# Kernel tuning notes

Measured on AMD Instinct MI355X. Metric: run time of the kernel, lower is better.

Reference implementation:

```python
import jax, jax.numpy as jnp
from jax import lax
import numpy as np

DN = ('NCDHW', 'OIDHW', 'NCDHW')
SLOPE = 0.01   # nn.LeakyReLU default negative_slope
EPS = 1e-5     # nn.BatchNorm1d default eps


def _conv(x, w, s, p):
    return lax.conv_general_dilated(x, w, (s, s, s), [(p, p)] * 3,
                                    dimension_numbers=DN)


def _tconv(x, w):
    # ConvTranspose3d(k=4, s=2, p=1) == conv with lhs_dilation=2,
    # pad = k-1-p = 2, spatially flipped kernel. w is (C_out, C_in, 4,4,4).
    return lax.conv_general_dilated(x, jnp.flip(w, (2, 3, 4)), (1, 1, 1),
                                    [(2, 2)] * 3, lhs_dilation=(2, 2, 2),
                                    dimension_numbers=DN)


def _bcast(v):
    return v[None, :, None, None, None]


def _masked_bn(y, m, g, b):
    # BatchNorm1d over ACTIVE voxels only (spconv stores only active sites).
    cnt = jnp.maximum(jnp.sum(m), 1.0)
    mean = jnp.sum(y * m, axis=(0, 2, 3, 4)) / cnt
    var = jnp.sum(jnp.square(y - _bcast(mean)) * m, axis=(0, 2, 3, 4)) / cnt
    yhat = (y - _bcast(mean)) * _bcast(lax.rsqrt(var + EPS))
    return (yhat * _bcast(g) + _bcast(b)) * m


def _block(x, m, w, b, g, be, transpose):
    # spconv SparseConv(Transpose)3d -> LeakyReLU -> BatchNorm1d, emulated
    # densely: x is zero off the active set m; output active set is the
    # dilation of m by the kernel footprint; bias/activation/BN touch only
    # active sites.
    ones_k = jnp.ones((1, 1, 4, 4, 4), x.dtype)
    if transpose:
        y = _tconv(x, w)
        m2 = (_tconv(m, ones_k) > 0).astype(x.dtype)
    else:
        y = _conv(x, w, 2, 1)
        m2 = (_conv(m, ones_k, 2, 1) > 0).astype(x.dtype)
    y = (y + _bcast(b)) * m2
    y = jnp.where(y >= 0, y, SLOPE * y)  # LeakyReLU (preserves zeros)
    return _masked_bn(y, m2, g, be), m2


def setup_inputs() -> dict:
    key = jax.random.key(0)
    ks = jax.random.split(key, 16)
    B, C, D = 2, 4, 64
    c = 32          # chans
    pred_dim = 32

    def w_init(k, shape):
        scale = 1.0 / float(np.sqrt(np.prod(shape[1:])))
        return jax.random.normal(k, shape, jnp.float32) * scale

    def b_init(k, n):
        return jax.random.normal(k, (n,), jnp.float32) * 0.01

    inp = {
        'feat': jax.random.normal(ks[0], (B, C, D, D, D), jnp.float32),
        'mask': jax.random.uniform(ks[1], (B, 1, D, D, D), jnp.float32),
        # down: [C->c, c->2c, 2c->4c], k=4 s=2 p=1
        'w1': w_init(ks[2], (c, C, 4, 4, 4)),
        'b1': b_init(ks[3], c),
        'g1': jnp.ones((c,), jnp.float32), 'be1': jnp.zeros((c,), jnp.float32),
        'w2': w_init(ks[4], (2 * c, c, 4, 4, 4)),
        'b2': b_init(ks[5], 2 * c),
        'g2': jnp.ones((2 * c,), jnp.float32), 'be2': jnp.zeros((2 * c,), jnp.float32),
        'w3': w_init(ks[6], (4 * c, 2 * c, 4, 4, 4)),
        'b3': b_init(ks[7], 4 * c),
        'g3': jnp.ones((4 * c,), jnp.float32), 'be3': jnp.zeros((4 * c,), jnp.float32),
        # up: [4c->4c, 4c->2c] (no skip-concat in the executed forward)
        'tw1': w_init(ks[8], (4 * c, 4 * c, 4, 4, 4)),
        'tb1': b_init(ks[9], 4 * c),
        'tg1': jnp.ones((4 * c,), jnp.float32), 'tbe1': jnp.zeros((4 * c,), jnp.float32),
        'tw2': w_init(ks[10], (2 * c, 4 * c, 4, 4, 4)),
        'tb2': b_init(ks[11], 2 * c),
        'tg2': jnp.ones((2 * c,), jnp.float32), 'tbe2': jnp.zeros((2 * c,), jnp.float32),
        # final dense 1x1x1 Conv3d: 2c -> pred_dim
        'fw': w_init(ks[12], (pred_dim, 2 * c, 1, 1, 1)),
        'fb': b_init(ks[13], pred_dim),
    }
    return inp


def reference(feat, mask, w1, b1, g1, be1, w2, b2, g2, be2, w3, b3, g3, be3,
              tw1, tb1, tg1, tbe1, tw2, tb2, tg2, tbe2, fw, fb):
    m = (mask > 0.5).astype(feat.dtype)
    x = feat * m  # gather of active voxel features == dense zero-fill
    x, m = _block(x, m, w1, b1, g1, be1, False)   # 64^3 -> 32^3
    x, m = _block(x, m, w2, b2, g2, be2, False)   # 32^3 -> 16^3
    x, m = _block(x, m, w3, b3, g3, be3, False)   # 16^3 -> 8^3
    x, m = _block(x, m, tw1, tb1, tg1, tbe1, True)  # 8^3 -> 16^3
    x, m = _block(x, m, tw2, tb2, tg2, tbe2, True)  # 16^3 -> 32^3
    # ToDense() then dense 1x1x1 Conv3d (bias applied everywhere)
    return _conv(x, fw, 1, 0) + _bcast(fb)
```

## Files before the change

### kernel.cpp

```cpp
#include <hip/hip_runtime.h>
#include <hip/hip_bf16.h>

#define DEV static __device__ __forceinline__

typedef unsigned short ushort;
typedef __attribute__((ext_vector_type(8))) short short8;
typedef __attribute__((ext_vector_type(8))) ushort ushort8;
typedef __attribute__((ext_vector_type(4))) ushort ushortx4;
typedef __attribute__((ext_vector_type(4))) float accv;

DEV ushort f2bf(float f) {
    __hip_bfloat16 h = __float2bfloat16(f);
    return reinterpret_cast<ushort&>(h);
}

__device__ float    g_sred[5 * 128 * 32];
__device__ float    g_part1[128 * 96];
__device__ float    g_part5[64 * 192];
__device__ float    g_y1[2097152];
__device__ __align__(16) ushort g_y1b[2097152];
__device__ float    g_m1[65536];
__device__ float    g_y2[524288];
__device__ __align__(16) ushort g_y2b[524288];
__device__ float    g_m2[8192];
__device__ float    g_y3[131072];
__device__ __align__(16) ushort g_y3b[131072];
__device__ float    g_m3[1024];
__device__ float    g_t1[1048576];
__device__ __align__(16) ushort g_t1b[1048576];
__device__ float    g_mt1[8192];
__device__ float    g_mt2[65536];
__device__ float    g_t2[4194304];
__device__ __align__(16) ushort g_x0b[2097152];
__device__ float    g_p2[4194304];
__device__ float    g_p3[4194304];
__device__ float    g_p4[8388608];
__device__ __align__(16) ushort g_wb1[8192];
__device__ __align__(16) ushort g_wb2[131072];
__device__ __align__(16) ushort g_wb3[524288];
__device__ __align__(16) ushort g_wb4[1048576];
__device__ __align__(16) ushort g_wb5[524288];
__device__ float    g_fwt[2048];

__global__ __launch_bounds__(256)
void prep_all_kernel(const float* __restrict__ w1, const float* __restrict__ fw,
                     const float* __restrict__ w2, const float* __restrict__ w3,
                     const float* __restrict__ tw1, const float* __restrict__ tw2,
                     const float* __restrict__ feat, const float* __restrict__ mask) {
    int blk = blockIdx.x, tid = threadIdx.x;
    if (blk < 96) {
        int idx = blk * 256 + tid;
        if (idx < 20480) g_sred[idx] = 0.f;
        if (idx < 12288) g_part1[idx] = 0.f;
        if (idx < 12288) g_part5[idx] = 0.f;
        if (idx < 8192) {
            int co = idx >> 8, r = idx & 255;
            int tap = r >> 2, ci = r & 3;
            g_wb1[idx] = f2bf(w1[co * 256 + ci * 64 + tap]);
        }
        if (idx < 2048) { int co = idx >> 6, kg = idx & 63; g_fwt[kg * 32 + co] = fw[idx]; }
    } else if (blk < 608) {
        int idx = (blk - 96) * 256 + tid;
        int co = idx / 2048, r = idx % 2048;
        int ci = r >> 6, tap = r & 63;
        g_wb2[(size_t)co * 2048 + tap * 32 + ci] = f2bf(w2[idx]);
    } else if (blk < 2656) {
        int idx = (blk - 608) * 256 + tid;
        int co = idx / 4096, r = idx % 4096;
        int ci = r >> 6, tap = r & 63;
        g_wb3[(size_t)co * 4096 + tap * 64 + ci] = f2bf(w3[idx]);
    } else if (blk < 6752) {
        int idx = (blk - 2656) * 256 + tid;
        int co = idx / 8192, r = idx % 8192;
        int ci = r >> 6, t64 = r & 63;
        int kd = t64 >> 4, kh = (t64 >> 2) & 3, kw = t64 & 3;
        int pd = (3 - kd) & 1, td = (3 - kd) >> 1;
        int ph = (3 - kh) & 1, th = (3 - kh) >> 1;
        int pw = (3 - kw) & 1, tw = (3 - kw) >> 1;
        int parity = pd * 4 + ph * 2 + pw, t = td * 4 + th * 2 + tw;
        g_wb4[(((size_t)parity * 128 + co) * 8 + t) * 128 + ci] = f2bf(tw1[idx]);
    } else if (blk < 8800) {
        int idx = (blk - 6752) * 256 + tid;
        int co = idx / 8192, r = idx % 8192;
        int ci = r >> 6, t64 = r & 63;
        int kd = t64 >> 4, kh = (t64 >> 2) & 3, kw = t64 & 3;
        int pd = (3 - kd) & 1, td = (3 - kd) >> 1;
        int ph = (3 - kh) & 1, th = (3 - kh) >> 1;
        int pw = (3 - kw) & 1, tw = (3 - kw) >> 1;
        int parity = pd * 4 + ph * 2 + pw, t = td * 4 + th * 2 + tw;
        g_wb5[(((size_t)parity * 64 + co) * 8 + t) * 128 + ci] = f2bf(tw2[idx]);
    } else if (blk < 10848) {
        int idx = (blk - 8800) * 256 + tid;
        int b = idx >> 18, v = idx & 0x3FFFF;
        float mv = mask[idx] > 0.5f ? 1.f : 0.f;
        ushort pk[4];
#pragma unroll
        for (int c = 0; c < 4; c++) pk[c] = f2bf(feat[((b * 4 + c) << 18) + v] * mv);
        *(ushortx4*)&g_x0b[(size_t)idx * 4] = (ushortx4){pk[0], pk[1], pk[2], pk[3]};
    } else {
        int idx = (blk - 10848) * 256 + tid;
        int b = idx >> 15, v = idx & 0x7FFF;
        int od = v >> 10, rem = v & 1023;
        int oh = rem >> 5, ow = rem & 31;
        const float* mp = mask + ((size_t)b << 18);
        float acc = 0.f;
        for (int kd = 0; kd < 4; kd++) {
            int id = 2 * od - 1 + kd;
            if ((unsigned)id >= 64u) continue;
            for (int kh = 0; kh < 4; kh++) {
                int ih = 2 * oh - 1 + kh;
                if ((unsigned)ih >= 64u) continue;
                const float* row = mp + ((size_t)id * 64 + ih) * 64;
                for (int kw = 0; kw < 4; kw++) {
                    int iw = 2 * ow - 1 + kw;
                    if ((unsigned)iw < 64u && row[iw] > 0.5f) acc += 1.f;
                }
            }
        }
        g_m1[idx] = acc > 0.f ? 1.f : 0.f;
    }
}

DEV void mask_down_blk(const float* mprev, float* mout, int logDin, int logDo, int blk) {
    int Din = 1 << logDin, Do = 1 << logDo;
    int idx = blk * 256 + threadIdx.x;
    int b = idx >> (3 * logDo), v = idx & ((1 << (3 * logDo)) - 1);
    int od = v >> (2 * logDo), rem = v & ((1 << (2 * logDo)) - 1);
    int oh = rem >> logDo, ow = rem & (Do - 1);
    const float* mp = mprev + ((size_t)b << (3 * logDin));
    float acc = 0.f;
    for (int kd = 0; kd < 4; kd++) {
        int id = 2 * od - 1 + kd;
        if ((unsigned)id >= (unsigned)Din) continue;
        for (int kh = 0; kh < 4; kh++) {
            int ih = 2 * oh - 1 + kh;
            if ((unsigned)ih >= (unsigned)Din) continue;
            const float* row = mp + ((size_t)id * Din + ih) * Din;
            for (int kw = 0; kw < 4; kw++) {
                int iw = 2 * ow - 1 + kw;
                if ((unsigned)iw < (unsigned)Din) acc += row[iw];
            }
        }
    }
    mout[idx] = acc > 0.f ? 1.f : 0.f;
}

DEV void mask_up_blk(const float* mprev, float* mout, int logDin, int logDo, int blk) {
    int Din = 1 << logDin, Do = 1 << logDo;
    int idx = blk * 256 + threadIdx.x;
    int b = idx >> (3 * logDo), v = idx & ((1 << (3 * logDo)) - 1);
    int od = v >> (2 * logDo), rem = v & ((1 << (2 * logDo)) - 1);
    int oh = rem >> logDo, ow = rem & (Do - 1);
    const float* mp = mprev + ((size_t)b << (3 * logDin));
    float acc = 0.f;
    for (int kd = 0; kd < 4; kd++) {
        int u = od + kd - 2; if (u < 0 || (u & 1)) continue;
        int id = u >> 1; if (id >= Din) continue;
        for (int kh = 0; kh < 4; kh++) {
            int uh = oh + kh - 2; if (uh < 0 || (uh & 1)) continue;
            int ih = uh >> 1; if (ih >= Din) continue;
            const float* row = mp + ((size_t)id * Din + ih) * Din;
            for (int kw = 0; kw < 4; kw++) {
                int uw = ow + kw - 2; if (uw < 0 || (uw & 1)) continue;
                int iw = uw >> 1; if (iw >= Din) continue;
                acc += row[iw];
            }
        }
    }
    mout[idx] = acc > 0.f ? 1.f : 0.f;
}

template<int MODE, int MT, int NT, int CIN, int COUT, int LOGDI, int LOGDO, int SPLITK,
         int KT, bool STATS = false>
DEV void mfma_gemm_body(const ushort* __restrict__ xb, const ushort* __restrict__ wb,
                        float* __restrict__ y,
                        const float* __restrict__ bias = nullptr,
                        const float* __restrict__ m2 = nullptr,
                        float* __restrict__ part = nullptr) {
    constexpr int K  = (MODE == 1) ? CIN * 8 : CIN * 64;
    constexpr int KSEG = K / SPLITK;
    constexpr int OCT = KT / 8;
    constexpr int LOGOCT = (KT == 32) ? 2 : 3;
    constexpr int KKN = KT / 32;
    constexpr int LDA = KT + 8;
    constexpr int MTW = MT / 32, NTW = NT / 32;
    constexpr int AR = MT * OCT / 256, BR = NT * OCT / 256;
    constexpr int LCIN = (CIN == 32) ? 5 : ((CIN == 64) ? 6 : 7);
    constexpr int Din = 1 << LOGDI, Do = 1 << LOGDO;
    constexpr int DvoxI = 1 << (3 * LOGDI), DvoxO = 1 << (3 * LOGDO);

    __shared__ __align__(16) ushort As[2][MT * LDA];
    __shared__ __align__(16) ushort Bs[2][NT * LDA];
    __shared__ float st[STATS ? COUT * 3 : 1];

    const int tid = threadIdx.x;
    const int bx = blockIdx.x;
    int pd = 0, ph = 0, pw = 0, ks = 0;
    const ushort* wp = wb;
    if constexpr (MODE == 1) {
        int z = blockIdx.z;
        pd = (z >> 2) & 1; ph = (z >> 1) & 1; pw = z & 1; ks = z >> 3;
        wp = wb + (size_t)(z & 7) * COUT * CIN * 8;
    } else {
        ks = blockIdx.z;
    }

    const int wv = tid >> 6, lane = tid & 63;
    const int mw = wv & 1, nw = wv >> 1;
    const int lr = lane & 15, quad = lane >> 4;

    if constexpr (STATS) {
        for (int i = tid; i < COUT * 3; i += 256) st[i] = 0.f;
    }

    int rB[BR], dB[BR], hB[BR], wBv[BR];
#pragma unroll
    for (int r = 0; r < BR; r++) {
        int slot = r * 256 + tid;
        int n = slot >> LOGOCT;
        int vg = bx * NT + n;
        if constexpr (MODE == 0) {
            rB[r] = vg >> (3 * LOGDO);
            int vv = vg & (DvoxO - 1);
            dB[r] = 2 * (vv >> (2 * LOGDO)) - 1;
            hB[r] = 2 * ((vv >> LOGDO) & (Do - 1)) - 1;
            wBv[r] = 2 * (vv & (Do - 1)) - 1;
        } else {
            rB[r] = vg >> (3 * LOGDI);
            int vv = vg & (DvoxI - 1);
            dB[r] = (vv >> (2 * LOGDI)) + pd - 1;
            hB[r] = ((vv >> LOGDI) & (Din - 1)) + ph - 1;
            wBv[r] = (vv & (Din - 1)) + pw - 1;
        }
    }

    auto gatherA = [&](int kt, ushort8* pa) {
#pragma unroll
        for (int r = 0; r < AR; r++) {
            int slot = r * 256 + tid;
            int m = slot >> LOGOCT, oct = slot & (OCT - 1);
            pa[r] = *(const ushort8*)&wp[(size_t)m * K + kt + oct * 8];
        }
    };
    auto gatherB = [&](int kt, ushort8* pb) {
#pragma unroll
        for (int r = 0; r < BR; r++) {
            int oct = (r * 256 + tid) & (OCT - 1);
            int kk0 = kt + oct * 8;
            int tap = kk0 >> LCIN;
            int ci0 = kk0 & (CIN - 1);
            int id_d, ih_d, iw_d;
            if constexpr (MODE == 0) { id_d = tap >> 4; ih_d = (tap >> 2) & 3; iw_d = tap & 3; }
            else                     { id_d = (tap >> 2) & 1; ih_d = (tap >> 1) & 1; iw_d = tap & 1; }
            int id = dB[r] + id_d, ih = hB[r] + ih_d, iw = wBv[r] + iw_d;
            ushort8 v = (ushort8){0, 0, 0, 0, 0, 0, 0, 0};
            if ((unsigned)id < (unsigned)Din && (unsigned)ih < (unsigned)Din &&
                (unsigned)iw < (unsigned)Din)
                v = *(const ushort8*)&xb[((size_t)rB[r] * DvoxI +
                                          (id << (2 * LOGDI)) + (ih << LOGDI) + iw) * CIN + ci0];
            pb[r] = v;
        }
    };
    auto stage = [&](int buf, ushort8* a, ushort8* b) {
#pragma unroll
        for (int r = 0; r < AR; r++) {
            int slot = r * 256 + tid;
            int m = slot >> LOGOCT, oct = slot & (OCT - 1);
            *(ushort8*)&As[buf][m * LDA + oct * 8] = a[r];
        }
#pragma unroll
        for (int r = 0; r < BR; r++) {
            int slot = r * 256 + tid;
            int n = slot >> LOGOCT, oct = slot & (OCT - 1);
            *(ushort8*)&Bs[buf][n * LDA + oct * 8] = b[r];
        }
    };

    accv acc[MTW][NTW];
#pragma unroll
    for (int mt = 0; mt < MTW; mt++)
#pragma unroll
        for (int nt = 0; nt < NTW; nt++) acc[mt][nt] = (accv){0.f, 0.f, 0.f, 0.f};

    const int kbeg = ks * KSEG, kend = kbeg + KSEG;
    ushort8 pa[AR], pb[BR], qa[AR], qb[BR];
    gatherA(kbeg, pa);
    gatherB(kbeg, pb);
    stage(0, pa, pb);
    __syncthreads();

    int cur = 0;
    for (int kt = kbeg; kt < kend; kt += KT) {
        bool more = (kt + KT) < kend;
        if (more) { gatherA(kt + KT, qa); gatherB(kt + KT, qb); }

        short8 af[MTW][KKN], bfr[NTW][KKN];
#pragma unroll
        for (int mt = 0; mt < MTW; mt++)
#pragma unroll
            for (int kk = 0; kk < KKN; kk++)
                af[mt][kk] = *(const short8*)&As[cur][((mw * MTW + mt) * 16 + lr) * LDA +
                                                     kk * 32 + quad * 8];
#pragma unroll
        for (int nt = 0; nt < NTW; nt++)
#pragma unroll
            for (int kk = 0; kk < KKN; kk++)
                bfr[nt][kk] = *(const short8*)&Bs[cur][((nw * NTW + nt) * 16 + lr) * LDA +
                                                      kk * 32 + quad * 8];
#pragma unroll
        for (int kk = 0; kk < KKN; kk++)
#pragma unroll
            for (int mt = 0; mt < MTW; mt++)
#pragma unroll
                for (int nt = 0; nt < NTW; nt++)
                    acc[mt][nt] = __builtin_amdgcn_mfma_f32_16x16x32_bf16(
                        af[mt][kk], bfr[nt][kk], acc[mt][nt], 0, 0, 0);
        if (more) {
            stage(cur ^ 1, qa, qb);
            __syncthreads();
            cur ^= 1;
        }
    }

    float* yp = y + (size_t)ks * (2 * COUT * DvoxO);
    float sacc[MTW][4], s2acc[MTW][4], bco[MTW][4];
    float mvs = 0.f;
    if constexpr (STATS) {
#pragma unroll
        for (int mt = 0; mt < MTW; mt++)
#pragma unroll
            for (int r = 0; r < 4; r++) {
                sacc[mt][r] = 0.f; s2acc[mt][r] = 0.f;
                bco[mt][r] = bias[(mw * MTW + mt) * 16 + quad * 4 + r];
            }
    }
#pragma unroll
    for (int nt = 0; nt < NTW; nt++) {
        int vg = bx * NT + (nw * NTW + nt) * 16 + lr;
        int b, vvox;
        if constexpr (MODE == 1) {
            b = vg >> (3 * LOGDI);
            int vv = vg & (DvoxI - 1);
            int odp = vv >> (2 * LOGDI), ohp = (vv >> LOGDI) & (Din - 1), owp = vv & (Din - 1);
            vvox = ((2 * odp + pd) << (2 * LOGDO)) + ((2 * ohp + ph) << LOGDO) + (2 * owp + pw);
        } else {
            b = vg >> (3 * LOGDO);
            vvox = vg & (DvoxO - 1);
        }
        float mv = 0.f;
        if constexpr (STATS) {
            mv = m2[((size_t)b << (3 * LOGDO)) + vvox];
            mvs += mv;
        }
        size_t base = (((size_t)b * COUT) << (3 * LOGDO)) + vvox;
#pragma unroll
        for (int mt = 0; mt < MTW; mt++) {
#pragma unroll
            for (int r = 0; r < 4; r++) {
                int co = (mw * MTW + mt) * 16 + quad * 4 + r;
                float v = acc[mt][nt][r];
                yp[base + ((size_t)co << (3 * LOGDO))] = v;
                if constexpr (STATS) {
                    float yv = (v + bco[mt][r]) * mv;
                    yv = yv >= 0.f ? yv : 0.01f * yv;
                    sacc[mt][r] += yv; s2acc[mt][r] += yv * yv;
                }
            }
        }
    }

    if constexpr (STATS) {
#pragma unroll
        for (int mt = 0; mt < MTW; mt++)
#pragma unroll
            for (int r = 0; r < 4; r++) {
                float s = sacc[mt][r], s2 = s2acc[mt][r];
#pragma unroll
                for (int o = 8; o; o >>= 1) {
                    s  += __shfl_xor(s, o, 16);
                    s2 += __shfl_xor(s2, o, 16);
                }
                if (lr == 0) {
                    int co = (mw * MTW + mt) * 16 + quad * 4 + r;
                    atomicAdd(&st[co * 3 + 0], s);
                    atomicAdd(&st[co * 3 + 1], s2);
                }
            }
        float ms = mvs;
#pragma unroll
        for (int o = 8; o; o >>= 1) ms += __shfl_xor(ms, o, 16);
        if (lr == 0) {
#pragma unroll
            for (int mt = 0; mt < MTW; mt++)
#pragma unroll
                for (int r = 0; r < 4; r++)
                    atomicAdd(&st[((mw * MTW + mt) * 16 + quad * 4 + r) * 3 + 2], ms);
        }
        __syncthreads();
        int bucket = bx & 63;
        for (int i = tid; i < COUT * 3; i += 256)
            atomicAdd(&part[bucket * COUT * 3 + i], st[i]);
    }
}

__global__ __launch_bounds__(256)
void conv2_kernel() { mfma_gemm_body<0, 64, 64, 32, 64, 5, 4, 4, 64>(g_y1b, g_wb2, g_p2); }
__global__ __launch_bounds__(256)
void conv3_kernel() { mfma_gemm_body<0, 128, 64, 64, 128, 4, 3, 32, 64>(g_y2b, g_wb3, g_p3); }
__global__ __launch_bounds__(256)
void conv4_kernel() { mfma_gemm_body<1, 128, 64, 128, 128, 3, 4, 4, 64>(g_y3b, g_wb4, g_p4); }
__global__ __launch_bounds__(256)
void conv5_kernel(const float* __restrict__ b5) {
    mfma_gemm_body<1, 64, 128, 128, 64, 4, 5, 1, 64, true>(g_t1b, g_wb5, g_t2,
                                                           b5, g_mt2, g_part5);
}

__global__ __launch_bounds__(256)
void conv1_kernel(const float* __restrict__ bias) {
    constexpr int LDA = 40;
    __shared__ __align__(16) ushort As[32 * LDA];
    __shared__ __align__(16) ushort Bs[64 * LDA];
    __shared__ float st[96];
    const int tid = threadIdx.x, bx = blockIdx.x;
    const int wv = tid >> 6, lane = tid & 63;
    const int lr = lane & 15, quad = lane >> 4;

    if (tid < 96) st[tid] = 0.f;

    const int nB = tid >> 2, octB = tid & 3;
    const int vgB = bx * 64 + nB;
    const int bB = vgB >> 15, vB = vgB & 32767;
    const int odB = vB >> 10, ohB = (vB >> 5) & 31, owB = vB & 31;

    auto gatherA = [&](int kt, ushort8& pa) {
        if (tid < 128) {
            int m = tid >> 2, oct = tid & 3;
            pa = *(const ushort8*)&g_wb1[m * 256 + kt + oct * 8];
        }
    };
    auto gatherB = [&](int kt, ushort8& pb) {
        int kg0 = kt + octB * 8;
        int t0 = kg0 >> 2;
        int kd = t0 >> 4, kh = (t0 >> 2) & 3, kw0 = t0 & 3;
        int id = 2 * odB - 1 + kd;
        int ih = 2 * ohB - 1 + kh;
        int iw0 = 2 * owB - 1 + kw0;
        ushort8 v = (ushort8){0, 0, 0, 0, 0, 0, 0, 0};
        if ((unsigned)id < 64u && (unsigned)ih < 64u) {
            const ushort* base = g_x0b + ((((size_t)bB << 18) + (id << 12) + (ih << 6)) << 2);
            if (iw0 >= 0 && iw0 + 1 < 64) {
                v = *(const ushort8*)&base[iw0 << 2];
            } else {
                if ((unsigned)iw0 < 64u) {
                    ushortx4 h = *(const ushortx4*)&base[iw0 << 2];
                    v[0] = h[0]; v[1] = h[1]; v[2] = h[2]; v[3] = h[3];
                }
                if ((unsigned)(iw0 + 1) < 64u) {
                    ushortx4 h = *(const ushortx4*)&base[(iw0 + 1) << 2];
                    v[4] = h[0]; v[5] = h[1]; v[6] = h[2]; v[7] = h[3];
                }
            }
        }
        pb = v;
    };

    accv acc[2];
    acc[0] = (accv){0.f, 0.f, 0.f, 0.f};
    acc[1] = (accv){0.f, 0.f, 0.f, 0.f};
    ushort8 pa, pb, qa, qb;
    gatherA(0, pa); gatherB(0, pb);

    for (int kt = 0; kt < 256; kt += 32) {
        __syncthreads();
        if (tid < 128) { int m = tid >> 2, oct = tid & 3; *(ushort8*)&As[m * LDA + oct * 8] = pa; }
        *(ushort8*)&Bs[nB * LDA + octB * 8] = pb;
        __syncthreads();
        bool more = kt < 224;
        if (more) { gatherA(kt + 32, qa); gatherB(kt + 32, qb); }

        short8 b8 = *(const short8*)&Bs[(wv * 16 + lr) * LDA + quad * 8];
#pragma unroll
        for (int mt = 0; mt < 2; mt++) {
            short8 a8 = *(const short8*)&As[(mt * 16 + lr) * LDA + quad * 8];
            acc[mt] = __builtin_amdgcn_mfma_f32_16x16x32_bf16(a8, b8, acc[mt], 0, 0, 0);
        }
        if (more) { pa = qa; pb = qb; }
    }

    int vg = bx * 64 + wv * 16 + lr;
    int b = vg >> 15, off = vg & 32767;
    float mv = g_m1[((size_t)b << 15) + off];
    float sacc[2][4], s2acc[2][4];
#pragma unroll
    for (int mt = 0; mt < 2; mt++) {
#pragma unroll
        for (int r = 0; r < 4; r++) {
            int co = mt * 16 + quad * 4 + r;
            float yv = (acc[mt][r] + bias[co]) * mv;
            yv = yv >= 0.f ? yv : 0.01f * yv;
            g_y1[(((size_t)(b * 32 + co)) << 15) + off] = yv;
            sacc[mt][r] = yv; s2acc[mt][r] = yv * yv;
        }
    }
#pragma unroll
    for (int mt = 0; mt < 2; mt++) {
#pragma unroll
        for (int r = 0; r < 4; r++) {
            float s = sacc[mt][r], s2 = s2acc[mt][r];
#pragma unroll
            for (int o = 8; o; o >>= 1) {
                s  += __shfl_xor(s, o, 16);
                s2 += __shfl_xor(s2, o, 16);
            }
            if (lr == 0) {
                int co = mt * 16 + quad * 4 + r;
                atomicAdd(&st[co * 3 + 0], s);
                atomicAdd(&st[co * 3 + 1], s2);
            }
        }
    }
    float ms = mv;
#pragma unroll
    for (int o = 8; o; o >>= 1) ms += __shfl_xor(ms, o, 16);
    if (lr == 0) {
#pragma unroll
        for (int mt = 0; mt < 2; mt++)
#pragma unroll
            for (int r = 0; r < 4; r++)
                atomicAdd(&st[(mt * 16 + quad * 4 + r) * 3 + 2], ms);
    }
    __syncthreads();
    if (tid < 96) atomicAdd(&g_part1[(bx & 127) * 96 + tid], st[tid]);
}

__global__ __launch_bounds__(256)
void final_kernel(const float* __restrict__ fb, const float* __restrict__ b5,
                  const float* __restrict__ tg2, const float* __restrict__ tbe2,
                  float* __restrict__ out) {
    __shared__ float As[1024];
    __shared__ float Bs[2048];
    __shared__ float sc5[64], sh5[64], bb5[64];
    const int tid = threadIdx.x, tc = tid & 15, tv = tid >> 4;
    const int bx = blockIdx.x;

    if (tid < 64) {
        float s0 = 0.f, s1 = 0.f, cnt = 0.f;
#pragma unroll 4
        for (int bkt = 0; bkt < 64; bkt++) {
            const float* p = g_part5 + bkt * 192 + tid * 3;
            s0 += p[0]; s1 += p[1]; cnt += p[2];
        }
        float n = fmaxf(cnt, 1.f);
        float mean = s0 / n;
        float var = fmaxf(s1 / n - mean * mean, 0.f);
        float rstd = rsqrtf(var + 1e-5f);
        float s = tg2[tid] * rstd;
        sc5[tid] = s; sh5[tid] = tbe2[tid] - mean * s; bb5[tid] = b5[tid];
    }

    float acc[2][4] = {{0.f}};
    for (int kt = 0; kt < 64; kt += 32) {
        __syncthreads();
#pragma unroll
        for (int e = 0; e < 4; e++) As[e * 256 + tid] = g_fwt[kt * 32 + e * 256 + tid];
#pragma unroll
        for (int e = 0; e < 8; e++) {
            int j = e * 256 + tid;
            int kk = j >> 6, n = j & 63;
            int kg = kt + kk;
            int vg = bx * 64 + n;
            int b = vg >> 15, v = vg & 32767;
            float raw = g_t2[(((size_t)(b * 64 + kg)) << 15) + v];
            float mv = g_mt2[((size_t)b << 15) + v];
            float t = (raw + bb5[kg]) * mv;
            t = t >= 0.f ? t : 0.01f * t;
            Bs[kk * 64 + n] = (t * sc5[kg] + sh5[kg]) * mv;
        }
        __syncthreads();
#pragma unroll
        for (int kk = 0; kk < 32; kk++) {
            float2 a2 = *(const float2*)&As[kk * 32 + tc * 2];
            float4 b4 = *(const float4*)&Bs[kk * 64 + tv * 4];
            float a[2] = {a2.x, a2.y};
            float bb[4] = {b4.x, b4.y, b4.z, b4.w};
#pragma unroll
            for (int r = 0; r < 2; r++)
#pragma unroll
                for (int c = 0; c < 4; c++) acc[r][c] = fmaf(a[r], bb[c], acc[r][c]);
        }
    }
#pragma unroll
    for (int r = 0; r < 2; r++) {
        int co = tc * 2 + r;
        float bv = fb[co];
#pragma unroll
        for (int c = 0; c < 4; c++) {
            int vg = bx * 64 + tv * 4 + c;
            int b = vg >> 15, v = vg & 32767;
            out[(((size_t)(b * 32 + co)) << 15) + v] = acc[r][c] + bv;
        }
    }
}

DEV void red3_and_atomic(float s, float s2, float sm, float* sred, int co) {
#pragma unroll
    for (int off = 32; off; off >>= 1) {
        s  += __shfl_down(s, off, 64);
        s2 += __shfl_down(s2, off, 64);
        sm += __shfl_down(sm, off, 64);
    }
    __shared__ float red[12];
    int lane = threadIdx.x & 63, wvi = threadIdx.x >> 6;
    if (!lane) { red[wvi] = s; red[4 + wvi] = s2; red[8 + wvi] = sm; }
    __syncthreads();
    if (!threadIdx.x) {
        atomicAdd(&sred[co * 32 + 0], red[0] + red[1] + red[2] + red[3]);
        atomicAdd(&sred[co * 32 + 1], red[4] + red[5] + red[6] + red[7]);
        atomicAdd(&sred[co * 32 + 2], red[8] + red[9] + red[10] + red[11]);
    }
}

template<int COUT, int LOGDO, int SPLITK, int ITERS, bool WRITE>
DEV void post_body(const float* __restrict__ bias, const float* __restrict__ m2,
                   const float* p, float* y, float* sred) {
    constexpr int Dvox = 1 << (3 * LOGDO);
    constexpr size_t STR = (size_t)2 * COUT * Dvox;
    constexpr int LOGC = (COUT == 128) ? 7 : ((COUT == 64) ? 6 : 5);
    int base = blockIdx.x * (ITERS * 256);
    int co = (base >> (3 * LOGDO)) & (COUT - 1);
    float s = 0.f, s2 = 0.f, sm = 0.f;
#pragma unroll
    for (int it = 0; it < ITERS; it++) {
        int idx = base + it * 256 + threadIdx.x;
        int v = idx & (Dvox - 1);
        int b = idx >> (3 * LOGDO + LOGC);
        float sum = 0.f;
#pragma unroll
        for (int k = 0; k < SPLITK; k++) sum += p[k * STR + idx];
        float mv = m2[((size_t)b << (3 * LOGDO)) + v];
        float yv = (sum + bias[co]) * mv;
        yv = yv >= 0.f ? yv : 0.01f * yv;
        if constexpr (WRITE) y[idx] = yv;
        s += yv; s2 += yv * yv; sm += mv;
    }
    red3_and_atomic(s, s2, sm, sred, co);
}

__global__ __launch_bounds__(256) void post2_kernel(const float* b) { post_body<64, 4, 4, 1, true>(b, g_m2, g_p2, g_y2, g_sred + 4096); }
__global__ __launch_bounds__(256) void post3_kernel(const float* b) { post_body<128, 3, 32, 1, true>(b, g_m3, g_p3, g_y3, g_sred + 8192); }
__global__ __launch_bounds__(256) void post4_kernel(const float* b) { post_body<128, 4, 4, 2, true>(b, g_mt1, g_p4, g_t1, g_sred + 12288); }

template<int LOGC, int LOGD, int PART>
DEV void bn_fused_body(const float* __restrict__ y, ushort* __restrict__ out,
                       const float* __restrict__ sred, const float* __restrict__ gm,
                       const float* __restrict__ be, const float* __restrict__ m2,
                       int blk) {
    constexpr int C = 1 << LOGC, Dvox = 1 << LOGD;
    __shared__ float sc[C], sh[C];
    int tid = threadIdx.x;
    if (tid < C) {
        float s0, s1, cnt;
        if constexpr (PART > 0) {
            s0 = 0.f; s1 = 0.f; cnt = 0.f;
#pragma unroll 4
            for (int bkt = 0; bkt < PART; bkt++) {
                const float* p = sred + bkt * C * 3 + tid * 3;
                s0 += p[0]; s1 += p[1]; cnt += p[2];
            }
        } else {
            s0 = sred[tid * 32]; s1 = sred[tid * 32 + 1]; cnt = sred[tid * 32 + 2];
        }
        float n = fmaxf(cnt, 1.f);
        float mean = s0 / n;
        float var = fmaxf(s1 / n - mean * mean, 0.f);
        float rstd = rsqrtf(var + 1e-5f);
        float s = gm[tid] * rstd;
        sc[tid] = s; sh[tid] = be[tid] - mean * s;
    }
    __syncthreads();
    int gv = blk * 256 + tid;
    int b = gv >> LOGD, vox = gv & (Dvox - 1);
    float mv = m2[gv];
    const float* yp = y + (((size_t)b << LOGC) << LOGD) + vox;
    ushort* op = out + (size_t)gv * C;
#pragma unroll
    for (int c0 = 0; c0 < C; c0 += 8) {
        ushort pk[8];
#pragma unroll
        for (int j = 0; j < 8; j++) {
            int c = c0 + j;
            float val = yp[(size_t)c << LOGD];
            pk[j] = f2bf((val * sc[c] + sh[c]) * mv);
        }
        *(ushort8*)&op[c0] = (ushort8){pk[0], pk[1], pk[2], pk[3], pk[4], pk[5], pk[6], pk[7]};
    }
}

__global__ __launch_bounds__(256)
void bn1_kernel(const float* g, const float* be) {
    if (blockIdx.x < 256) bn_fused_body<5, 15, 128>(g_y1, g_y1b, g_part1, g, be, g_m1, blockIdx.x);
    else mask_down_blk(g_m1, g_m2, 5, 4, blockIdx.x - 256);
}
__global__ __launch_bounds__(256)
void bn2_kernel(const float* g, const float* be) {
    if (blockIdx.x < 32) bn_fused_body<6, 12, 0>(g_y2, g_y2b, g_sred + 4096, g, be, g_m2, blockIdx.x);
    else mask_down_blk(g_m2, g_m3, 4, 3, blockIdx.x - 32);
}
__global__ __launch_bounds__(256)
void bn3_kernel(const float* g, const float* be) {
    if (blockIdx.x < 4) bn_fused_body<7, 9, 0>(g_y3, g_y3b, g_sred + 8192, g, be, g_m3, blockIdx.x);
    else mask_up_blk(g_m3, g_mt1, 3, 4, blockIdx.x - 4);
}
__global__ __launch_bounds__(256)
void bn4_kernel(const float* g, const float* be) {
    if (blockIdx.x < 32) bn_fused_body<7, 12, 0>(g_t1, g_t1b, g_sred + 12288, g, be, g_mt1, blockIdx.x);
    else mask_up_blk(g_mt1, g_mt2, 4, 5, blockIdx.x - 32);
}


extern "C" void kernel_launch(void* const* d_in, const int* in_sizes, int n_in,
                              void* d_out, int out_size, void* d_ws, size_t ws_size,
                              hipStream_t stream) {
    (void)in_sizes; (void)n_in; (void)out_size; (void)d_ws; (void)ws_size;
    const float* feat = (const float*)d_in[0];
    const float* mask = (const float*)d_in[1];
    const float* w1  = (const float*)d_in[2];
    const float* b1  = (const float*)d_in[3];
    const float* g1  = (const float*)d_in[4];
    const float* be1 = (const float*)d_in[5];
    const float* w2  = (const float*)d_in[6];
    const float* b2  = (const float*)d_in[7];
    const float* g2  = (const float*)d_in[8];
    const float* be2 = (const float*)d_in[9];
    const float* w3  = (const float*)d_in[10];
    const float* b3  = (const float*)d_in[11];
    const float* g3  = (const float*)d_in[12];
    const float* be3 = (const float*)d_in[13];
    const float* tw1 = (const float*)d_in[14];
    const float* tb1 = (const float*)d_in[15];
    const float* tg1 = (const float*)d_in[16];
    const float* tbe1= (const float*)d_in[17];
    const float* tw2 = (const float*)d_in[18];
    const float* tb2 = (const float*)d_in[19];
    const float* tg2 = (const float*)d_in[20];
    const float* tbe2= (const float*)d_in[21];
    const float* fw  = (const float*)d_in[22];
    const float* fb  = (const float*)d_in[23];

    prep_all_kernel<<<11104, 256, 0, stream>>>(w1, fw, w2, w3, tw1, tw2, feat, mask);

    conv1_kernel<<<1024, 256, 0, stream>>>(b1);
    bn1_kernel<<<288, 256, 0, stream>>>(g1, be1);

    conv2_kernel<<<dim3(128, 1, 4), 256, 0, stream>>>();
    post2_kernel<<<2048, 256, 0, stream>>>(b2);
    bn2_kernel<<<36, 256, 0, stream>>>(g2, be2);

    conv3_kernel<<<dim3(16, 1, 32), 256, 0, stream>>>();
    post3_kernel<<<512, 256, 0, stream>>>(b3);
    bn3_kernel<<<36, 256, 0, stream>>>(g3, be3);

    conv4_kernel<<<dim3(16, 1, 32), 256, 0, stream>>>();
    post4_kernel<<<2048, 256, 0, stream>>>(tb1);
    bn4_kernel<<<288, 256, 0, stream>>>(tg1, tbe1);

    conv5_kernel<<<dim3(64, 1, 8), 256, 0, stream>>>(tb2);

    final_kernel<<<1024, 256, 0, stream>>>(fb, tb2, tg2, tbe2, (float*)d_out);
}
```

Baseline: 264.5 us.

## Store conv1 and conv5 activations as bf16 and retile conv3 split-K

Conv1 and conv5 now write their post-LeakyReLU activations as bf16 instead of fp32, and the BN and final kernels read them back as bf16. Conv5's bias and activation move into the GEMM epilogue, so the final kernel only applies the BN affine. This halves the intermediate traffic for two large tensors, at the cost of rounding pre-BN values to bf16 (BN statistics are still accumulated in fp32). Conv3 also switches to a narrower N tile with less split-K, which changes the grid and the partial-sum count that post3 reduces.

```diff
diff --git a/kernel.cpp b/kernel.cpp
--- a/kernel.cpp
+++ b/kernel.cpp
@@ -14,10 +14,12 @@
     return reinterpret_cast<ushort&>(h);
 }
 
+DEV float bf2f(ushort u) { return __uint_as_float((unsigned)u << 16); }
+
 __device__ float    g_sred[5 * 128 * 32];
 __device__ float    g_part1[128 * 96];
 __device__ float    g_part5[64 * 192];
-__device__ float    g_y1[2097152];
+__device__ __align__(16) ushort g_y1h[2097152];
 __device__ __align__(16) ushort g_y1b[2097152];
 __device__ float    g_m1[65536];
 __device__ float    g_y2[524288];
@@ -30,7 +32,7 @@
 __device__ __align__(16) ushort g_t1b[1048576];
 __device__ float    g_mt1[8192];
 __device__ float    g_mt2[65536];
-__device__ float    g_t2[4194304];
+__device__ __align__(16) ushort g_t2b[4194304];
 __device__ __align__(16) ushort g_x0b[2097152];
 __device__ float    g_p2[4194304];
 __device__ float    g_p3[4194304];
@@ -171,7 +173,7 @@
 }
 
 template<int MODE, int MT, int NT, int CIN, int COUT, int LOGDI, int LOGDO, int SPLITK,
-         int KT, bool STATS = false>
+         int KT, bool STATS = false, bool OUTBF = false>
 DEV void mfma_gemm_body(const ushort* __restrict__ xb, const ushort* __restrict__ wb,
                         float* __restrict__ y,
                         const float* __restrict__ bias = nullptr,
@@ -359,11 +361,15 @@
             for (int r = 0; r < 4; r++) {
                 int co = (mw * MTW + mt) * 16 + quad * 4 + r;
                 float v = acc[mt][nt][r];
-                yp[base + ((size_t)co << (3 * LOGDO))] = v;
+                size_t oidx = base + ((size_t)co << (3 * LOGDO));
                 if constexpr (STATS) {
                     float yv = (v + bco[mt][r]) * mv;
                     yv = yv >= 0.f ? yv : 0.01f * yv;
+                    if constexpr (OUTBF) ((ushort*)yp)[oidx] = f2bf(yv);
+                    else                 yp[oidx] = v;
                     sacc[mt][r] += yv; s2acc[mt][r] += yv * yv;
+                } else {
+                    yp[oidx] = v;
                 }
             }
         }
@@ -406,13 +412,13 @@
 __global__ __launch_bounds__(256)
 void conv2_kernel() { mfma_gemm_body<0, 64, 64, 32, 64, 5, 4, 4, 64>(g_y1b, g_wb2, g_p2); }
 __global__ __launch_bounds__(256)
-void conv3_kernel() { mfma_gemm_body<0, 128, 64, 64, 128, 4, 3, 32, 64>(g_y2b, g_wb3, g_p3); }
+void conv3_kernel() { mfma_gemm_body<0, 128, 32, 64, 128, 4, 3, 16, 64>(g_y2b, g_wb3, g_p3); }
 __global__ __launch_bounds__(256)
 void conv4_kernel() { mfma_gemm_body<1, 128, 64, 128, 128, 3, 4, 4, 64>(g_y3b, g_wb4, g_p4); }
 __global__ __launch_bounds__(256)
 void conv5_kernel(const float* __restrict__ b5) {
-    mfma_gemm_body<1, 64, 128, 128, 64, 4, 5, 1, 64, true>(g_t1b, g_wb5, g_t2,
-                                                           b5, g_mt2, g_part5);
+    mfma_gemm_body<1, 64, 128, 128, 64, 4, 5, 1, 64, true, true>(
+        g_t1b, g_wb5, (float*)g_t2b, b5, g_mt2, g_part5);
 }
 
 __global__ __launch_bounds__(256)
@@ -498,7 +504,7 @@
             int co = mt * 16 + quad * 4 + r;
             float yv = (acc[mt][r] + bias[co]) * mv;
             yv = yv >= 0.f ? yv : 0.01f * yv;
-            g_y1[(((size_t)(b * 32 + co)) << 15) + off] = yv;
+            g_y1h[(((size_t)(b * 32 + co)) << 15) + off] = f2bf(yv);
             sacc[mt][r] = yv; s2acc[mt][r] = yv * yv;
         }
     }
@@ -534,12 +540,12 @@
 }
 
 __global__ __launch_bounds__(256)
-void final_kernel(const float* __restrict__ fb, const float* __restrict__ b5,
+void final_kernel(const float* __restrict__ fb,
                   const float* __restrict__ tg2, const float* __restrict__ tbe2,
                   float* __restrict__ out) {
     __shared__ float As[1024];
     __shared__ float Bs[2048];
-    __shared__ float sc5[64], sh5[64], bb5[64];
+    __shared__ float sc5[64], sh5[64];
     const int tid = threadIdx.x, tc = tid & 15, tv = tid >> 4;
     const int bx = blockIdx.x;
 
@@ -555,7 +561,7 @@
         float var = fmaxf(s1 / n - mean * mean, 0.f);
         float rstd = rsqrtf(var + 1e-5f);
         float s = tg2[tid] * rstd;
-        sc5[tid] = s; sh5[tid] = tbe2[tid] - mean * s; bb5[tid] = b5[tid];
+        sc5[tid] = s; sh5[tid] = tbe2[tid] - mean * s;
     }
 
     float acc[2][4] = {{0.f}};
@@ -570,11 +576,9 @@
             int kg = kt + kk;
             int vg = bx * 64 + n;
             int b = vg >> 15, v = vg & 32767;
-            float raw = g_t2[(((size_t)(b * 64 + kg)) << 15) + v];
+            float yv = bf2f(g_t2b[(((size_t)(b * 64 + kg)) << 15) + v]);
             float mv = g_mt2[((size_t)b << 15) + v];
-            float t = (raw + bb5[kg]) * mv;
-            t = t >= 0.f ? t : 0.01f * t;
-            Bs[kk * 64 + n] = (t * sc5[kg] + sh5[kg]) * mv;
+            Bs[kk * 64 + n] = (yv * sc5[kg] + sh5[kg]) * mv;
         }
         __syncthreads();
 #pragma unroll
@@ -647,11 +651,11 @@
 }
 
 __global__ __launch_bounds__(256) void post2_kernel(const float* b) { post_body<64, 4, 4, 1, true>(b, g_m2, g_p2, g_y2, g_sred + 4096); }
-__global__ __launch_bounds__(256) void post3_kernel(const float* b) { post_body<128, 3, 32, 1, true>(b, g_m3, g_p3, g_y3, g_sred + 8192); }
+__global__ __launch_bounds__(256) void post3_kernel(const float* b) { post_body<128, 3, 16, 1, true>(b, g_m3, g_p3, g_y3, g_sred + 8192); }
 __global__ __launch_bounds__(256) void post4_kernel(const float* b) { post_body<128, 4, 4, 2, true>(b, g_mt1, g_p4, g_t1, g_sred + 12288); }
 
-template<int LOGC, int LOGD, int PART>
-DEV void bn_fused_body(const float* __restrict__ y, ushort* __restrict__ out,
+template<int LOGC, int LOGD, int PART, typename YT>
+DEV void bn_fused_body(const YT* __restrict__ y, ushort* __restrict__ out,
                        const float* __restrict__ sred, const float* __restrict__ gm,
                        const float* __restrict__ be, const float* __restrict__ m2,
                        int blk) {
@@ -681,7 +685,7 @@
     int gv = blk * 256 + tid;
     int b = gv >> LOGD, vox = gv & (Dvox - 1);
     float mv = m2[gv];
-    const float* yp = y + (((size_t)b << LOGC) << LOGD) + vox;
+    const YT* yp = y + (((size_t)b << LOGC) << LOGD) + vox;
     ushort* op = out + (size_t)gv * C;
 #pragma unroll
     for (int c0 = 0; c0 < C; c0 += 8) {
@@ -689,7 +693,9 @@
 #pragma unroll
         for (int j = 0; j < 8; j++) {
             int c = c0 + j;
-            float val = yp[(size_t)c << LOGD];
+            float val;
+            if constexpr (sizeof(YT) == 2) val = bf2f((ushort)yp[(size_t)c << LOGD]);
+            else                           val = yp[(size_t)c << LOGD];
             pk[j] = f2bf((val * sc[c] + sh[c]) * mv);
         }
         *(ushort8*)&op[c0] = (ushort8){pk[0], pk[1], pk[2], pk[3], pk[4], pk[5], pk[6], pk[7]};
@@ -698,7 +704,7 @@
 
 __global__ __launch_bounds__(256)
 void bn1_kernel(const float* g, const float* be) {
-    if (blockIdx.x < 256) bn_fused_body<5, 15, 128>(g_y1, g_y1b, g_part1, g, be, g_m1, blockIdx.x);
+    if (blockIdx.x < 256) bn_fused_body<5, 15, 128>(g_y1h, g_y1b, g_part1, g, be, g_m1, blockIdx.x);
     else mask_down_blk(g_m1, g_m2, 5, 4, blockIdx.x - 256);
 }
 __global__ __launch_bounds__(256)
@@ -756,7 +762,7 @@
     post2_kernel<<<2048, 256, 0, stream>>>(b2);
     bn2_kernel<<<36, 256, 0, stream>>>(g2, be2);
 
-    conv3_kernel<<<dim3(16, 1, 32), 256, 0, stream>>>();
+    conv3_kernel<<<dim3(32, 1, 16), 256, 0, stream>>>();
     post3_kernel<<<512, 256, 0, stream>>>(b3);
     bn3_kernel<<<36, 256, 0, stream>>>(g3, be3);
 
@@ -766,5 +772,5 @@
 
     conv5_kernel<<<dim3(64, 1, 8), 256, 0, stream>>>(tb2);
 
-    final_kernel<<<1024, 256, 0, stream>>>(fb, tb2, tg2, tbe2, (float*)d_out);
-}
+    final_kernel<<<1024, 256, 0, stream>>>(fb, tg2, tbe2, (float*)d_out);
+}
```

Measured after the change: 257.9 us, median of 2. 1.03x faster.
